# Kernel optimization log

Hardware: AMD Instinct MI355X
Metric: run time of the kernel (lower is better)

## Reference

```python
import jax, jax.numpy as jnp
import numpy as np

B, T, H = 256, 512, 1024


def setup_inputs() -> dict:
    key = jax.random.key(0)
    ks = jax.random.split(key, 11)
    s = 1.0 / np.sqrt(H)
    u = lambda k, shape: jax.random.uniform(k, shape, jnp.float32, -s, s)
    return {
        "x": jax.random.normal(ks[0], (B, T), jnp.float32),
        "W_ih1": u(ks[1], (4 * H, 1)),
        "W_hh1": u(ks[2], (4 * H, H)),
        "b_ih1": u(ks[3], (4 * H,)),
        "b_hh1": u(ks[4], (4 * H,)),
        "W_ih2": u(ks[5], (4 * H, H)),
        "W_hh2": u(ks[6], (4 * H, H)),
        "b_ih2": u(ks[7], (4 * H,)),
        "b_hh2": u(ks[8], (4 * H,)),
        "W_out": u(ks[9], (1, H)),
        "b_out": u(ks[10], (1,)),
        "future": 0,
    }


def _lstm_cell(x, h, c, W_ih, W_hh, b):
    # PyTorch LSTMCell gate order: i, f, g, o
    gates = x @ W_ih.T + h @ W_hh.T + b
    i, f, g, o = jnp.split(gates, 4, axis=-1)
    c_new = jax.nn.sigmoid(f) * c + jax.nn.sigmoid(i) * jnp.tanh(g)
    h_new = jax.nn.sigmoid(o) * jnp.tanh(c_new)
    return h_new, c_new


def reference(x, W_ih1, W_hh1, b_ih1, b_hh1, W_ih2, W_hh2, b_ih2, b_hh2, W_out, b_out, future):
    Bn = x.shape[0]
    Hd = W_hh1.shape[1]
    b1 = b_ih1 + b_hh1
    b2 = b_ih2 + b_hh2

    def step(carry, x_t):
        h1, c1, h2, c2 = carry
        h1, c1 = _lstm_cell(x_t, h1, c1, W_ih1, W_hh1, b1)
        h2, c2 = _lstm_cell(h1, h2, c2, W_ih2, W_hh2, b2)
        out = h2 @ W_out.T + b_out  # [B, 1]
        return (h1, c1, h2, c2), out

    xs = x.T[:, :, None]  # [T, B, 1]
    carry0 = tuple(jnp.zeros((Bn, Hd), x.dtype) for _ in range(4))
    carry, outs = jax.lax.scan(step, carry0, xs)  # outs: [T, B, 1]
    outputs = [outs[:, :, 0].T]  # [B, T]

    # closed-loop future prediction (future is a static Python int)
    out = outs[-1]
    for _ in range(future):
        carry, out = step(carry, out)
        outputs.append(out)
    return jnp.concatenate(outputs, axis=1)
```

## Files before the change

kernel.cpp:

```cpp
#include <hip/hip_runtime.h>
#include <hip/hip_cooperative_groups.h>
#include <math.h>

namespace cg = cooperative_groups;

#define Bsz 256
#define Tsz 512
#define GSTR 258

using half8 = __attribute__((ext_vector_type(8))) _Float16;
using half4 = __attribute__((ext_vector_type(4))) _Float16;
using f32x4 = __attribute__((ext_vector_type(4))) float;

#define MFMA_V(acc, a, b) (acc) = __builtin_amdgcn_mfma_f32_16x16x32_f16((a), (b), (acc), 0, 0, 0)
#define INV2048 (1.0f / 2048.0f)

__device__ __forceinline__ float sigm(float v)   { return 1.0f / (1.0f + expf(-v)); }
__device__ __forceinline__ float tanh_f(float v) { float e = expf(2.0f * v); return 1.0f - 2.0f / (e + 1.0f); }

__device__ __forceinline__ void split8(const float* p, half8& hi, half8& lo) {
    float4 v0 = *(const float4*)p, v1 = *(const float4*)(p + 4);
    float vv[8] = {v0.x, v0.y, v0.z, v0.w, v1.x, v1.y, v1.z, v1.w};
    #pragma unroll
    for (int j = 0; j < 8; ++j) {
        hi[j] = (_Float16)vv[j];
        lo[j] = (_Float16)((vv[j] - (float)hi[j]) * 2048.0f);
    }
}

__device__ __forceinline__ void grid_barrier(unsigned* bar0, unsigned* bar1,
                                             int bx, unsigned target16) {
    __syncthreads();
    if (threadIdx.x == 0) {
        unsigned old = __hip_atomic_fetch_add(&bar0[(bx & 15) << 5], 1u,
                                              __ATOMIC_ACQ_REL, __HIP_MEMORY_SCOPE_AGENT);
        if ((old & 15u) == 15u)
            __hip_atomic_fetch_add(bar1, 1u, __ATOMIC_ACQ_REL, __HIP_MEMORY_SCOPE_AGENT);
        while (__hip_atomic_load(bar1, __ATOMIC_RELAXED, __HIP_MEMORY_SCOPE_AGENT) < target16)
            __builtin_amdgcn_s_sleep(2);
        (void)__hip_atomic_load(bar1, __ATOMIC_ACQUIRE, __HIP_MEMORY_SCOPE_AGENT);
    }
    __syncthreads();
}

__global__ __launch_bounds__(512, 2) void lstm_persist(
    const float* __restrict__ x,
    const float* __restrict__ W_ih1, const float* __restrict__ W_hh1,
    const float* __restrict__ b_ih1, const float* __restrict__ b_hh1,
    const float* __restrict__ W_ih2, const float* __restrict__ W_hh2,
    const float* __restrict__ b_ih2, const float* __restrict__ b_hh2,
    const float* __restrict__ W_out, const float* __restrict__ b_out,
    float* __restrict__ out, char* __restrict__ ws)
{
    __shared__ float gAcc[32 * GSTR];
    __shared__ float poArr[2 * GSTR];
    __shared__ float bp[32], wihp[32], woutp[8];
    __shared__ float bouts_s;

    cg::grid_group grid = cg::this_grid();

    const int tid  = threadIdx.x;
    const int lane = tid & 63;
    const int wv   = tid >> 6;
    const int m    = lane & 15;
    const int quad = lane >> 4;
    const int bx   = blockIdx.x;
    const bool isL2 = (bx >= 128);
    const int rg   = isL2 ? (bx - 128) : bx;
    const int HO   = rg << 3;

    float*    xT       = (float*)ws;
    _Float16* hswz     = (_Float16*)(ws + (512 << 10));
    float*    partials = (float*)(ws + (512 << 10) + (4 << 20));
    unsigned* bar0     = (unsigned*)(ws + (512 << 10) + (4 << 20) + (256 << 10));
    unsigned* bar1     = bar0 + 1024;

    #define HBUF(p, l, hl) (hswz + ((((p) << 2) | ((l) << 1) | (hl)) << 18))

    if (bx == 0) {
        if (tid < 16) bar0[tid << 5] = 0u;
        if (tid == 16) *bar1 = 0u;
    }
    if (tid < 32) {
        const int row = ((tid & 3) << 10) + HO + (tid >> 2);
        if (!isL2) {
            bp[tid]   = b_ih1[row] + b_hh1[row];
            wihp[tid] = W_ih1[row];
        } else {
            bp[tid] = b_ih2[row] + b_hh2[row];
            if (tid < 8) woutp[tid] = W_out[HO + tid];
        }
        if (tid == 0) bouts_s = b_out[0];
    }
    {
        const int gidx = bx * 512 + tid;
        *(float4*)((char*)hswz + (2u << 20) + (size_t)gidx * 16) = make_float4(0, 0, 0, 0);
        xT[gidx] = x[(gidx & 255) * Tsz + (gidx >> 8)];
    }

    grid.sync();

    const int b_ep = tid & 255, hg = tid >> 8;
    const int k0e  = HO + (hg << 2);
    const int wofs = ((b_ep >> 4) << 14) + ((k0e >> 5) << 9)
                   + (((b_ep & 15) | (((k0e >> 3) & 3) << 4)) << 3) + (k0e & 7);

    if (!isL2) {
        half8 wh[2][4], wl[2][4];
        #pragma unroll
        for (int mt = 0; mt < 2; ++mt) {
            const int pr = (mt << 4) + m;
            const size_t rw = (size_t)(((pr & 3) << 10) + HO + (pr >> 2)) << 10;
            #pragma unroll
            for (int kt = 0; kt < 4; ++kt) {
                const int k = (wv << 7) + (kt << 5) + (quad << 3);
                split8(W_hh1 + rw + k, wh[mt][kt], wl[mt][kt]);
            }
        }
        for (int idx = tid; idx < 8192; idx += 512) {
            const int p = idx >> 8, b = idx & 255;
            gAcc[p * GSTR + b] = bp[p] + xT[b] * wihp[p];
        }
        __syncthreads();
        float cr[4] = {0, 0, 0, 0};

        for (int it = 0; it <= Tsz; ++it) {
            const int parW = it & 1;
            const int parR = parW ^ 1;

            float xnext = 0.0f;
            if (it + 1 < Tsz) xnext = xT[((it + 1) << 8) + b_ep];

            if (wv == 0 && it >= 2) {
                const float* pp = partials + (parW << 15) + (bx << 7);
                float s = pp[lane] + pp[lane + 64];
                s += __shfl_xor(s, 32); s += __shfl_xor(s, 16); s += __shfl_xor(s, 8);
                s += __shfl_xor(s, 4);  s += __shfl_xor(s, 2);  s += __shfl_xor(s, 1);
                if (lane == 0) out[(bx << 9) + (it - 2)] = bouts_s + s;
            }

            if (it < Tsz) {
                const _Float16* bhB = HBUF(parR, 0, 0);
                const _Float16* blB = HBUF(parR, 0, 1);
                const int lo_off = (wv << 11) + (lane << 3);
                #pragma unroll 2
                for (int bi = 0; bi < 16; ++bi) {
                    const int btl = (bi + (wv << 1)) & 15;
                    const _Float16* ph = bhB + (btl << 14) + lo_off;
                    const _Float16* pl = blB + (btl << 14) + lo_off;
                    f32x4 a0[2] = {(f32x4){0,0,0,0}, (f32x4){0,0,0,0}};
                    f32x4 a1[2] = {(f32x4){0,0,0,0}, (f32x4){0,0,0,0}};
                    half8 bh = *(const half8*)ph;
                    half8 bl = *(const half8*)pl;
                    #pragma unroll
                    for (int kt = 0; kt < 4; ++kt) {
                        half8 bhN, blN;
                        if (kt < 3) {
                            bhN = *(const half8*)(ph + ((kt + 1) << 9));
                            blN = *(const half8*)(pl + ((kt + 1) << 9));
                        }
                        MFMA_V(a0[0], wh[0][kt], bh);
                        MFMA_V(a1[0], wh[0][kt], bl);
                        MFMA_V(a1[0], wl[0][kt], bh);
                        MFMA_V(a0[1], wh[1][kt], bh);
                        MFMA_V(a1[1], wh[1][kt], bl);
                        MFMA_V(a1[1], wl[1][kt], bh);
                        bh = bhN; bl = blN;
                    }
                    const int col = (btl << 4) + m;
                    #pragma unroll
                    for (int mt = 0; mt < 2; ++mt)
                        #pragma unroll
                        for (int r = 0; r < 4; ++r)
                            atomicAdd(&gAcc[((mt << 4) + (quad << 2) + r) * GSTR + col],
                                      a0[mt][r] + a1[mt][r] * INV2048);
                }
            }

            __syncthreads();

            if (it < Tsz) {
                half4 hhi, hlo;
                #pragma unroll
                for (int j = 0; j < 4; ++j) {
                    const int p = (hg << 4) + (j << 2);
                    const float gi = gAcc[(p + 0) * GSTR + b_ep];
                    const float gf = gAcc[(p + 1) * GSTR + b_ep];
                    const float gg = gAcc[(p + 2) * GSTR + b_ep];
                    const float go = gAcc[(p + 3) * GSTR + b_ep];
                    const float c  = sigm(gf) * cr[j] + sigm(gi) * tanh_f(gg);
                    cr[j] = c;
                    const float hn = sigm(go) * tanh_f(c);
                    hhi[j] = (_Float16)hn;
                    hlo[j] = (_Float16)((hn - (float)hhi[j]) * 2048.0f);
                }
                *(half4*)(HBUF(parW, 0, 0) + wofs) = hhi;
                *(half4*)(HBUF(parW, 0, 1) + wofs) = hlo;
                if (it + 1 < Tsz) {
                    #pragma unroll
                    for (int p = (hg << 4); p < (hg << 4) + 16; ++p)
                        gAcc[p * GSTR + b_ep] = bp[p] + xnext * wihp[p];
                }
            }

            grid_barrier(bar0, bar1, bx, 16u * (unsigned)(it + 1));
        }
    } else {
        half8 wh[2][8], wl[2][8];
        #pragma unroll
        for (int mt = 0; mt < 2; ++mt) {
            const int pr = (mt << 4) + m;
            const size_t rw = (size_t)(((pr & 3) << 10) + HO + (pr >> 2)) << 10;
            #pragma unroll
            for (int kt = 0; kt < 8; ++kt) {
                const int k = (wv << 8) + (kt << 5) + (quad << 3);
                const float* p = (k < 1024) ? (W_ih2 + rw + k)
                                            : (W_hh2 + rw + k - 1024);
                split8(p, wh[mt][kt], wl[mt][kt]);
            }
        }
        for (int idx = tid; idx < 8192; idx += 512) {
            const int p = idx >> 8, b = idx & 255;
            gAcc[p * GSTR + b] = bp[p];
        }
        __syncthreads();
        float cr[4] = {0, 0, 0, 0};

        for (int it = 0; it <= Tsz; ++it) {
            const int parW = it & 1;
            const int parR = parW ^ 1;

            if (wv == 0 && it >= 2) {
                const float* pp = partials + (parW << 15) + (bx << 7);
                float s = pp[lane] + pp[lane + 64];
                s += __shfl_xor(s, 32); s += __shfl_xor(s, 16); s += __shfl_xor(s, 8);
                s += __shfl_xor(s, 4);  s += __shfl_xor(s, 2);  s += __shfl_xor(s, 1);
                if (lane == 0) out[(bx << 9) + (it - 2)] = bouts_s + s;
            }

            if (it >= 1) {
                const bool hi2 = (wv >= 4);
                const _Float16* bhB = hi2 ? HBUF(parW, 1, 0) : HBUF(parR, 0, 0);
                const _Float16* blB = hi2 ? HBUF(parW, 1, 1) : HBUF(parR, 0, 1);
                const int lo_off = ((wv & 3) << 12) + (lane << 3);
                #pragma unroll 2
                for (int bi = 0; bi < 16; ++bi) {
                    const int btl = (bi + (wv << 1)) & 15;
                    const _Float16* ph = bhB + (btl << 14) + lo_off;
                    const _Float16* pl = blB + (btl << 14) + lo_off;
                    f32x4 a0[2] = {(f32x4){0,0,0,0}, (f32x4){0,0,0,0}};
                    f32x4 a1[2] = {(f32x4){0,0,0,0}, (f32x4){0,0,0,0}};
                    half8 bh = *(const half8*)ph;
                    half8 bl = *(const half8*)pl;
                    #pragma unroll
                    for (int kt = 0; kt < 8; ++kt) {
                        half8 bhN, blN;
                        if (kt < 7) {
                            bhN = *(const half8*)(ph + ((kt + 1) << 9));
                            blN = *(const half8*)(pl + ((kt + 1) << 9));
                        }
                        MFMA_V(a0[0], wh[0][kt], bh);
                        MFMA_V(a1[0], wh[0][kt], bl);
                        MFMA_V(a1[0], wl[0][kt], bh);
                        MFMA_V(a0[1], wh[1][kt], bh);
                        MFMA_V(a1[1], wh[1][kt], bl);
                        MFMA_V(a1[1], wl[1][kt], bh);
                        bh = bhN; bl = blN;
                    }
                    const int col = (btl << 4) + m;
                    #pragma unroll
                    for (int mt = 0; mt < 2; ++mt)
                        #pragma unroll
                        for (int r = 0; r < 4; ++r)
                            atomicAdd(&gAcc[((mt << 4) + (quad << 2) + r) * GSTR + col],
                                      a0[mt][r] + a1[mt][r] * INV2048);
                }
            }

            __syncthreads();

            if (it >= 1) {
                half4 hhi, hlo;
                float po = 0.0f;
                #pragma unroll
                for (int j = 0; j < 4; ++j) {
                    const int p = (hg << 4) + (j << 2);
                    const float gi = gAcc[(p + 0) * GSTR + b_ep];
                    const float gf = gAcc[(p + 1) * GSTR + b_ep];
                    const float gg = gAcc[(p + 2) * GSTR + b_ep];
                    const float go = gAcc[(p + 3) * GSTR + b_ep];
                    const float c  = sigm(gf) * cr[j] + sigm(gi) * tanh_f(gg);
                    cr[j] = c;
                    const float hn = sigm(go) * tanh_f(c);
                    hhi[j] = (_Float16)hn;
                    hlo[j] = (_Float16)((hn - (float)hhi[j]) * 2048.0f);
                    po += hn * woutp[(hg << 2) + j];
                }
                *(half4*)(HBUF(parR, 1, 0) + wofs) = hhi;
                *(half4*)(HBUF(parR, 1, 1) + wofs) = hlo;
                poArr[hg * GSTR + b_ep] = po;
                #pragma unroll
                for (int p = (hg << 4); p < (hg << 4) + 16; ++p)
                    gAcc[p * GSTR + b_ep] = bp[p];
            }
            __syncthreads();
            if (it >= 1 && tid < 256) {
                const float s = poArr[tid] + poArr[GSTR + tid];
                partials[(parR << 15) + (tid << 7) + rg] = s;
            }

            grid_barrier(bar0, bar1, bx, 16u * (unsigned)(it + 1));
        }
    }

    if (wv == 0) {
        const float* pp = partials + (1 << 15) + (bx << 7);
        float s = pp[lane] + pp[lane + 64];
        s += __shfl_xor(s, 32); s += __shfl_xor(s, 16); s += __shfl_xor(s, 8);
        s += __shfl_xor(s, 4);  s += __shfl_xor(s, 2);  s += __shfl_xor(s, 1);
        if (lane == 0) out[(bx << 9) + (Tsz - 1)] = bouts_s + s;
    }
    #undef HBUF
}

extern "C" void kernel_launch(void* const* d_in, const int* in_sizes, int n_in,
                              void* d_out, int out_size, void* d_ws, size_t ws_size,
                              hipStream_t stream)
{
    const float* x     = (const float*)d_in[0];
    const float* W_ih1 = (const float*)d_in[1];
    const float* W_hh1 = (const float*)d_in[2];
    const float* b_ih1 = (const float*)d_in[3];
    const float* b_hh1 = (const float*)d_in[4];
    const float* W_ih2 = (const float*)d_in[5];
    const float* W_hh2 = (const float*)d_in[6];
    const float* b_ih2 = (const float*)d_in[7];
    const float* b_hh2 = (const float*)d_in[8];
    const float* W_out = (const float*)d_in[9];
    const float* b_out = (const float*)d_in[10];
    float* out = (float*)d_out;
    char*  ws  = (char*)d_ws;

    void* args[] = {
        (void*)&x,
        (void*)&W_ih1, (void*)&W_hh1, (void*)&b_ih1, (void*)&b_hh1,
        (void*)&W_ih2, (void*)&W_hh2, (void*)&b_ih2, (void*)&b_hh2,
        (void*)&W_out, (void*)&b_out, (void*)&out, (void*)&ws,
    };
    hipLaunchCooperativeKernel((const void*)lstm_persist,
                               dim3(256), dim3(512), args, 0, stream);
}
```

Before: 51.74 ms.

## Replace grid barrier with XCC-leader two-phase barrier and relaxed atomics

Rewrites the per-timestep grid barrier. One leader block per XCC, identified through the hardware XCC_ID register, waits for the global arrival count and performs a single acquire-release atomic for its XCC. It then bumps a phase counter that every block spins on, followed by an explicit cache invalidate. The aim is to cut the per-block acq_rel fences and L2 writeback/invalidate traffic of every step. Launch bounds drop from 2 to 1 block per SIMD occupancy hint. Correctness now depends on the leader's fence ordering writes from every block in its XCC, so memory-ordering bugs are possible.

```diff
diff --git a/kernel.cpp b/kernel.cpp
--- a/kernel.cpp
+++ b/kernel.cpp
@@ -28,22 +28,32 @@
     }
 }
 
-__device__ __forceinline__ void grid_barrier(unsigned* bar0, unsigned* bar1,
-                                             int bx, unsigned target16) {
+__device__ __forceinline__ void step_barrier(unsigned* bar0, unsigned* bar1,
+                                             unsigned* phase2, unsigned* dummyv,
+                                             int bx, int isLead, unsigned xcc,
+                                             unsigned nLead, unsigned it1) {
     __syncthreads();
     if (threadIdx.x == 0) {
         unsigned old = __hip_atomic_fetch_add(&bar0[(bx & 15) << 5], 1u,
-                                              __ATOMIC_ACQ_REL, __HIP_MEMORY_SCOPE_AGENT);
+                                              __ATOMIC_RELAXED, __HIP_MEMORY_SCOPE_AGENT);
         if ((old & 15u) == 15u)
-            __hip_atomic_fetch_add(bar1, 1u, __ATOMIC_ACQ_REL, __HIP_MEMORY_SCOPE_AGENT);
-        while (__hip_atomic_load(bar1, __ATOMIC_RELAXED, __HIP_MEMORY_SCOPE_AGENT) < target16)
-            __builtin_amdgcn_s_sleep(2);
-        (void)__hip_atomic_load(bar1, __ATOMIC_ACQUIRE, __HIP_MEMORY_SCOPE_AGENT);
+            __hip_atomic_fetch_add(bar1, 1u, __ATOMIC_RELAXED, __HIP_MEMORY_SCOPE_AGENT);
+        if (isLead) {
+            while (__hip_atomic_load(bar1, __ATOMIC_RELAXED, __HIP_MEMORY_SCOPE_AGENT) < 16u * it1)
+                __builtin_amdgcn_s_sleep(1);
+            __hip_atomic_fetch_add(&dummyv[xcc << 5], 1u,
+                                   __ATOMIC_ACQ_REL, __HIP_MEMORY_SCOPE_AGENT);
+            __hip_atomic_fetch_add(phase2, 1u,
+                                   __ATOMIC_RELAXED, __HIP_MEMORY_SCOPE_AGENT);
+        }
+        while (__hip_atomic_load(phase2, __ATOMIC_RELAXED, __HIP_MEMORY_SCOPE_AGENT) < nLead * it1)
+            __builtin_amdgcn_s_sleep(1);
+        asm volatile("buffer_inv sc0" ::: "memory");
     }
     __syncthreads();
 }
 
-__global__ __launch_bounds__(512, 2) void lstm_persist(
+__global__ __launch_bounds__(512, 1) void lstm_persist(
     const float* __restrict__ x,
     const float* __restrict__ W_ih1, const float* __restrict__ W_hh1,
     const float* __restrict__ b_ih1, const float* __restrict__ b_hh1,
@@ -56,6 +66,7 @@
     __shared__ float poArr[2 * GSTR];
     __shared__ float bp[32], wihp[32], woutp[8];
     __shared__ float bouts_s;
+    __shared__ unsigned isLead_s, xcc_s, nLead_s;
 
     cg::grid_group grid = cg::this_grid();
 
@@ -74,13 +85,15 @@
     float*    partials = (float*)(ws + (512 << 10) + (4 << 20));
     unsigned* bar0     = (unsigned*)(ws + (512 << 10) + (4 << 20) + (256 << 10));
     unsigned* bar1     = bar0 + 1024;
+    unsigned* phase2   = bar0 + 1056;
+    unsigned* nLeadCt  = bar0 + 1057;
+    unsigned* claimA   = bar0 + 1088;
+    unsigned* dummyv   = bar0 + 1536;
 
     #define HBUF(p, l, hl) (hswz + ((((p) << 2) | ((l) << 1) | (hl)) << 18))
 
-    if (bx == 0) {
-        if (tid < 16) bar0[tid << 5] = 0u;
-        if (tid == 16) *bar1 = 0u;
-    }
+    if (bx == 0)
+        for (int i = tid; i < 2048; i += 512) bar0[i] = 0u;
     if (tid < 32) {
         const int row = ((tid & 3) << 10) + HO + (tid >> 2);
         if (!isL2) {
@@ -99,6 +112,26 @@
     }
 
     grid.sync();
+
+    if (tid == 0) {
+        unsigned xcc;
+        asm volatile("s_getreg_b32 %0, hwreg(HW_REG_XCC_ID)" : "=s"(xcc));
+        xcc &= 7u;
+        xcc_s = xcc;
+        unsigned old = __hip_atomic_fetch_add(&claimA[xcc << 5], 1u,
+                                              __ATOMIC_RELAXED, __HIP_MEMORY_SCOPE_AGENT);
+        isLead_s = (old == 0u);
+        if (old == 0u)
+            __hip_atomic_fetch_add(nLeadCt, 1u,
+                                   __ATOMIC_RELAXED, __HIP_MEMORY_SCOPE_AGENT);
+    }
+    grid.sync();
+    if (tid == 0)
+        nLead_s = __hip_atomic_load(nLeadCt, __ATOMIC_RELAXED, __HIP_MEMORY_SCOPE_AGENT);
+    __syncthreads();
+    const int      isLead = (int)isLead_s;
+    const unsigned xcc    = xcc_s;
+    const unsigned nLead  = nLead_s;
 
     const int b_ep = tid & 255, hg = tid >> 8;
     const int k0e  = HO + (hg << 2);
@@ -203,7 +236,8 @@
                 }
             }
 
-            grid_barrier(bar0, bar1, bx, 16u * (unsigned)(it + 1));
+            step_barrier(bar0, bar1, phase2, dummyv, bx, isLead, xcc, nLead,
+                         (unsigned)(it + 1));
         }
     } else {
         half8 wh[2][8], wl[2][8];
@@ -309,7 +343,8 @@
                 partials[(parR << 15) + (tid << 7) + rg] = s;
             }
 
-            grid_barrier(bar0, bar1, bx, 16u * (unsigned)(it + 1));
+            step_barrier(bar0, bar1, phase2, dummyv, bx, isLead, xcc, nLead,
+                         (unsigned)(it + 1));
         }
     }
 
```

Result: faster. 47.78 ms (-7.7%).
